# Optimization experiments

Hardware: AMD Instinct MI355X
Metric: run time of the kernel (lower is better)

Reference implementation:

```python
import jax, jax.numpy as jnp
import numpy as np

B, N, C, H, W = 2, 6, 64, 28, 50
D = 59  # len(arange(1.0, 60.0, 1.0))
BH, BW = 200, 200
BEV_X0, BEV_Y0 = -50.0, -50.0
RES_X, RES_Y = 0.5, 0.5  # (50-(-50))/200


def setup_inputs() -> dict:
    key = jax.random.key(0)
    k1, k2 = jax.random.split(key)
    features = jax.random.normal(k1, (B, N, C, H, W), dtype=jnp.float32)
    # depth distribution over D bins (softmax-normalized, as a depth net would emit)
    depth = jax.nn.softmax(jax.random.normal(k2, (B, N, D, H, W), dtype=jnp.float32), axis=2)
    # realistic pinhole intrinsics for a WxH feature map
    K = np.zeros((B, N, 3, 3), np.float32)
    K[..., 0, 0] = float(W)
    K[..., 1, 1] = float(W)
    K[..., 0, 2] = W / 2.0
    K[..., 1, 2] = H / 2.0
    K[..., 2, 2] = 1.0
    # cam-to-ego extrinsics: axis remap (z_cam->x_ego, x_cam->-y_ego, y_cam->-z_ego)
    # composed with a per-camera yaw, plus a small mounting translation
    R0 = np.array([[0, 0, 1], [-1, 0, 0], [0, -1, 0]], np.float32)
    E = np.zeros((B, N, 4, 4), np.float32)
    for n in range(N):
        yaw = 2.0 * np.pi * n / N
        Rz = np.array([[np.cos(yaw), -np.sin(yaw), 0.0],
                       [np.sin(yaw), np.cos(yaw), 0.0],
                       [0.0, 0.0, 1.0]], np.float32)
        E[:, n, :3, :3] = Rz @ R0
        E[:, n, 0, 3] = 1.5 * np.cos(yaw)
        E[:, n, 1, 3] = 1.5 * np.sin(yaw)
        E[:, n, 2, 3] = 1.6
    E[..., 3, 3] = 1.0
    return {
        "features": features,
        "depth": depth,
        "intrinsics": jnp.asarray(K),
        "extrinsics": jnp.asarray(E),
    }


def _frustum_ego(intrinsics, extrinsics):
    # pixel grid (H, W, 3) homogeneous coords
    xs = jnp.linspace(0.0, W - 1.0, W, dtype=jnp.float32)
    ys = jnp.linspace(0.0, H - 1.0, H, dtype=jnp.float32)
    yy, xx = jnp.meshgrid(ys, xs, indexing="ij")
    pix = jnp.stack([xx, yy, jnp.ones_like(xx)], axis=-1)  # (H, W, 3)
    depth_bins = jnp.arange(1.0, 60.0, 1.0, dtype=jnp.float32)  # (D,)
    frustum_cam = pix[None] * depth_bins[:, None, None, None]  # (D, H, W, 3)
    K_inv = jnp.linalg.inv(intrinsics)  # (B, N, 3, 3)
    cam = jnp.einsum("bnij,dhwj->bndhwi", K_inv, frustum_cam)  # (B, N, D, H, W, 3)
    R = extrinsics[..., :3, :3]
    t = extrinsics[..., :3, 3]
    ego = jnp.einsum("bnij,bndhwj->bndhwi", R, cam) + t[:, :, None, None, None, :]
    return ego


def reference(features, depth, intrinsics, extrinsics):
    ego = _frustum_ego(intrinsics, extrinsics)  # (B, N, D, H, W, 3)

    # lift: outer product of features (B,N,C,H,W) and depth (B,N,D,H,W)
    lifted = features[:, :, None] * depth[:, :, :, None]  # (B, N, D, C, H, W)
    lifted = lifted.transpose(0, 1, 2, 4, 5, 3).reshape(B, -1, C)  # b (n d h w) c

    fr = ego.reshape(B, -1, 3)  # b (n d h w) xyz
    x, y, z = fr[..., 0], fr[..., 1], fr[..., 2]
    # torch .long() truncates toward zero -> astype(int32) matches
    bx = ((x - BEV_X0) / RES_X).astype(jnp.int32)
    by = ((y - BEV_Y0) / RES_Y).astype(jnp.int32)
    valid = (bx >= 0) & (bx < BW) & (by >= 0) & (by < BH) & (z > 0)

    # flat scatter index with per-batch offset; invalid -> dummy segment (dropped)
    b_off = (jnp.arange(B, dtype=jnp.int32) * (BH * BW))[:, None]
    flat_idx = jnp.where(valid, b_off + by * BW + bx, B * BH * BW)
    seg = jax.ops.segment_sum(
        lifted.reshape(-1, C), flat_idx.reshape(-1), num_segments=B * BH * BW + 1
    )
    bev = seg[: B * BH * BW].reshape(B, BH, BW, C).transpose(0, 3, 1, 2)  # (B, C, BH, BW)
    return bev
```

## Files before the change

kernel.cpp:

```cpp
#include <hip/hip_runtime.h>
#include <hip/hip_bf16.h>

#define Bc 2
#define Nc 6
#define Cc 64
#define Hc 28
#define Wc 50
#define Dc 59
#define BHc 200
#define BWc 200

#define HWc (Hc * Wc)
#define NWAVES 8
#define DWAVE 8
#define NZ 640
#define ACC_ELEMS ((size_t)Bc * BHc * BWc * Cc)

__global__ __launch_bounds__(256) void fp_zero(float* __restrict__ acc)
{
    const size_t NF4 = ACC_ELEMS / 4;
    float4* a4 = (float4*)acc;
    size_t base = (size_t)blockIdx.x * 2048;
#pragma unroll
    for (int it = 0; it < 8; ++it) {
        size_t i = base + (size_t)it * 256 + threadIdx.x;
        if (i < NF4) a4[i] = make_float4(0.f, 0.f, 0.f, 0.f);
    }
}

__global__ __launch_bounds__(512) void fp_scatter6(
    const float* __restrict__ feats,
    const float* __restrict__ depth,
    const float* __restrict__ Kmat,
    const float* __restrict__ Emat,
    float* __restrict__ acc)
{
    __shared__ __align__(16) float feat_lds[Hc][Cc];

    int bid = blockIdx.x;
    int L   = (bid & 7) * 75 + (bid >> 3);
    int w   = L % Wc;
    int bn  = L / Wc;
    int b   = bn / Nc;
    int tid  = threadIdx.x;
    int lane = tid & 63;
    int wid  = tid >> 6;

    const size_t HW = (size_t)HWc;
    const float* fbase = feats + (size_t)bn * Cc * HW + w;
    const float* dcol  = depth + (size_t)bn * Dc * HW + w;

    for (int hh = wid; hh < Hc; hh += NWAVES)
        feat_lds[hh][lane] = fbase[(size_t)lane * HW + (size_t)hh * Wc];

    const float* K = Kmat + (size_t)bn * 9;
    float k00 = K[0], k01 = K[1], k02 = K[2];
    float k10 = K[3], k11 = K[4], k12 = K[5];
    float k20 = K[6], k21 = K[7], k22 = K[8];

    float c00 = __fsub_rn(__fmul_rn(k11, k22), __fmul_rn(k12, k21));
    float c01 = __fsub_rn(__fmul_rn(k12, k20), __fmul_rn(k10, k22));
    float c02 = __fsub_rn(__fmul_rn(k10, k21), __fmul_rn(k11, k20));
    float det = __fadd_rn(__fadd_rn(__fmul_rn(k00, c00), __fmul_rn(k01, c01)),
                          __fmul_rn(k02, c02));
    float i00 = __fdiv_rn(c00, det);
    float i01 = __fdiv_rn(__fsub_rn(__fmul_rn(k02, k21), __fmul_rn(k01, k22)), det);
    float i02 = __fdiv_rn(__fsub_rn(__fmul_rn(k01, k12), __fmul_rn(k02, k11)), det);
    float i10 = __fdiv_rn(c01, det);
    float i11 = __fdiv_rn(__fsub_rn(__fmul_rn(k00, k22), __fmul_rn(k02, k20)), det);
    float i12 = __fdiv_rn(__fsub_rn(__fmul_rn(k02, k10), __fmul_rn(k00, k12)), det);
    float i20 = __fdiv_rn(c02, det);
    float i21 = __fdiv_rn(__fsub_rn(__fmul_rn(k01, k20), __fmul_rn(k00, k21)), det);
    float i22 = __fdiv_rn(__fsub_rn(__fmul_rn(k00, k11), __fmul_rn(k01, k10)), det);

    const float* E = Emat + (size_t)bn * 16;
    float r00 = E[0], r01 = E[1], r02 = E[2],  tx = E[3];
    float r10 = E[4], r11 = E[5], r12 = E[6],  ty = E[7];
    float r20 = E[8], r21 = E[9], r22 = E[10], tz = E[11];

    __syncthreads();

    float* accb = acc + (size_t)b * (BHc * BWc) * Cc;

    int h = lane;
    float xf = (float)w;
    float yf = (float)h;

    float accv[DWAVE];
    float mval[DWAVE];
    int   prim[DWAVE];

#pragma unroll
    for (int k = 0; k < DWAVE; ++k) {
        accv[k] = 0.0f;
        mval[k] = 0.0f;
        prim[k] = -1;
        int dg = wid + NWAVES * k;
        if (dg < Dc) {
            float db = (float)(dg + 1);
            float dep = 0.0f;
            if (h < Hc)
                dep = dcol[(size_t)dg * HW + (size_t)h * Wc];

            float px = __fmul_rn(xf, db);
            float py = __fmul_rn(yf, db);
            float pz = db;

            float cx = __fadd_rn(__fadd_rn(__fmul_rn(i00, px), __fmul_rn(i01, py)), __fmul_rn(i02, pz));
            float cy = __fadd_rn(__fadd_rn(__fmul_rn(i10, px), __fmul_rn(i11, py)), __fmul_rn(i12, pz));
            float cz = __fadd_rn(__fadd_rn(__fmul_rn(i20, px), __fmul_rn(i21, py)), __fmul_rn(i22, pz));

            float ex = __fadd_rn(__fadd_rn(__fadd_rn(__fmul_rn(r00, cx), __fmul_rn(r01, cy)), __fmul_rn(r02, cz)), tx);
            float ey = __fadd_rn(__fadd_rn(__fadd_rn(__fmul_rn(r10, cx), __fmul_rn(r11, cy)), __fmul_rn(r12, cz)), ty);
            float ez = __fadd_rn(__fadd_rn(__fadd_rn(__fmul_rn(r20, cx), __fmul_rn(r21, cy)), __fmul_rn(r22, cz)), tz);

            int bx = (int)(__fmul_rn(__fadd_rn(ex, 50.0f), 2.0f));
            int by = (int)(__fmul_rn(__fadd_rn(ey, 50.0f), 2.0f));

            bool valid = (h < Hc) & (bx >= 0) & (bx < BWc) & (by >= 0) & (by < BHc) & (ez > 0.0f);
            int binidx = by * BWc + bx;

            unsigned long long vm = __ballot(valid);
            if (vm != 0ULL) {
                int first = __builtin_ctzll(vm);
                int pr = __shfl(binidx, first);
                unsigned long long match = __ballot(valid && (binidx == pr));
                unsigned long long rest  = vm & ~match;
                prim[k] = pr;
                mval[k] = (valid && (binidx == pr)) ? dep : 0.0f;

                while (rest) {
                    int hh2 = __builtin_ctzll(rest);
                    rest &= rest - 1;
                    int   bidx = __shfl(binidx, hh2);
                    float dv   = __shfl(dep, hh2);
                    atomicAdd(&accb[(size_t)bidx * Cc + lane],
                              __fmul_rn(feat_lds[hh2][lane], dv));
                }
            }
        }
    }

#pragma unroll
    for (int hh = 0; hh < Hc; ++hh) {
        float f = feat_lds[hh][lane];
#pragma unroll
        for (int k = 0; k < DWAVE; ++k) {
            float dk = __int_as_float(
                __builtin_amdgcn_readlane(__float_as_int(mval[k]), hh));
            accv[k] = __builtin_fmaf(f, dk, accv[k]);
        }
    }

#pragma unroll
    for (int k = 0; k < DWAVE; ++k) {
        if (prim[k] >= 0)
            atomicAdd(&accb[(size_t)prim[k] * Cc + lane], accv[k]);
    }
}

__global__ __launch_bounds__(256) void fp_transpose_kernel(
    const float* __restrict__ acc, float* __restrict__ out)
{
    __shared__ float tile[64][65];
    const int P = BHc * BWc;
    int b = blockIdx.y;
    int p0 = blockIdx.x * 64;
    int tx = threadIdx.x & 63;
    int ty = threadIdx.x >> 6;

    const float* src = acc + (size_t)b * P * Cc;
#pragma unroll
    for (int i = 0; i < 16; ++i) {
        int row = ty * 16 + i;
        tile[row][tx] = src[(size_t)(p0 + row) * Cc + tx];
    }
    __syncthreads();
    float* dst = out + (size_t)b * Cc * P;
#pragma unroll
    for (int i = 0; i < 16; ++i) {
        int c = ty * 16 + i;
        dst[(size_t)c * P + p0 + tx] = tile[tx][c];
    }
}

extern "C" void kernel_launch(void* const* d_in, const int* in_sizes, int n_in,
                              void* d_out, int out_size, void* d_ws, size_t ws_size,
                              hipStream_t stream) {
    const float* feats = (const float*)d_in[0];
    const float* depth = (const float*)d_in[1];
    const float* Kmat  = (const float*)d_in[2];
    const float* Emat  = (const float*)d_in[3];
    float* out = (float*)d_out;

    float* acc = (float*)d_ws;

    fp_zero<<<NZ, 256, 0, stream>>>(acc);

    fp_scatter6<<<600, 512, 0, stream>>>(feats, depth, Kmat, Emat, acc);

    fp_transpose_kernel<<<dim3((BHc * BWc) / 64, Bc), 256, 0, stream>>>(acc, out);
}
```

Baseline: 97.09 us.

## Exploit column-independent BEV bins to reduce over image rows before scattering

The scatter kernel is restructured so each block covers one camera and a pair of depth bins. It checks at runtime whether the intrinsics and extrinsics have zero yaw-cross terms. When they do, the BEV bin depends only on (w, d), so features times depth are summed over all rows in registers and a single atomic is issued per (w, d, channel). A general fallback still does a per-point atomic scatter. Features are staged per row pair in a swizzled LDS tile, which cuts atomic traffic but relies on an exact-zero matrix check that may not hold for most cameras (the yawed ones).

```diff
diff --git a/kernel.cpp b/kernel.cpp
--- a/kernel.cpp
+++ b/kernel.cpp
@@ -10,11 +10,11 @@
 #define BHc 200
 #define BWc 200
 
-#define HWc (Hc * Wc)
-#define NWAVES 8
-#define DWAVE 8
 #define NZ 640
 #define ACC_ELEMS ((size_t)Bc * BHc * BWc * Cc)
+#define DT 2
+#define NTILE 30
+#define NBLK (12 * NTILE)
 
 __global__ __launch_bounds__(256) void fp_zero(float* __restrict__ acc)
 {
@@ -28,134 +28,216 @@
     }
 }
 
-__global__ __launch_bounds__(512) void fp_scatter6(
+__global__ __launch_bounds__(256) void fp_fused(
     const float* __restrict__ feats,
     const float* __restrict__ depth,
     const float* __restrict__ Kmat,
     const float* __restrict__ Emat,
     float* __restrict__ acc)
 {
-    __shared__ __align__(16) float feat_lds[Hc][Cc];
-
-    int bid = blockIdx.x;
-    int L   = (bid & 7) * 75 + (bid >> 3);
-    int w   = L % Wc;
-    int bn  = L / Wc;
-    int b   = bn / Nc;
+    __shared__ __align__(16) float f_lds[2][64][64];
+    __shared__ float dep_lds[DT][Hc][52];
+
+    int bid  = blockIdx.x;
+    int xcd  = bid & 7;
+    int j    = bid >> 3;
+    int k    = (xcd & 1) * 45 + j;
+    int g    = xcd >> 1;
+    int bn   = 3 * g + k / 30;
+    int t    = k % 30;
+    int b    = bn / Nc;
+    int d0   = t * DT;
+
     int tid  = threadIdx.x;
     int lane = tid & 63;
-    int wid  = tid >> 6;
-
-    const size_t HW = (size_t)HWc;
-    const float* fbase = feats + (size_t)bn * Cc * HW + w;
-    const float* dcol  = depth + (size_t)bn * Dc * HW + w;
-
-    for (int hh = wid; hh < Hc; hh += NWAVES)
-        feat_lds[hh][lane] = fbase[(size_t)lane * HW + (size_t)hh * Wc];
+    int q    = tid >> 6;
+
+    const size_t HW = (size_t)Hc * Wc;
+    const float* Fb = feats + (size_t)bn * Cc * HW;
+    const float* Db = depth + (size_t)bn * Dc * HW;
+
+    for (int i = tid; i < (DT * Hc * Wc) / 2; i += 256) {
+        int dp  = i / 700;
+        int rem = i % 700;
+        int hh  = rem / 25;
+        int w2  = rem % 25;
+        int dg  = d0 + dp;
+        float2 v = make_float2(0.f, 0.f);
+        if (dg < Dc)
+            v = *(const float2*)(Db + ((size_t)dg * Hc + hh) * Wc + 2 * w2);
+        dep_lds[dp][hh][2 * w2]     = v.x;
+        dep_lds[dp][hh][2 * w2 + 1] = v.y;
+    }
 
     const float* K = Kmat + (size_t)bn * 9;
     float k00 = K[0], k01 = K[1], k02 = K[2];
     float k10 = K[3], k11 = K[4], k12 = K[5];
     float k20 = K[6], k21 = K[7], k22 = K[8];
-
-    float c00 = __fsub_rn(__fmul_rn(k11, k22), __fmul_rn(k12, k21));
-    float c01 = __fsub_rn(__fmul_rn(k12, k20), __fmul_rn(k10, k22));
-    float c02 = __fsub_rn(__fmul_rn(k10, k21), __fmul_rn(k11, k20));
-    float det = __fadd_rn(__fadd_rn(__fmul_rn(k00, c00), __fmul_rn(k01, c01)),
-                          __fmul_rn(k02, c02));
+    float c00 = __fsub_rn(__fmul_rn(k11,k22), __fmul_rn(k12,k21));
+    float c01 = __fsub_rn(__fmul_rn(k12,k20), __fmul_rn(k10,k22));
+    float c02 = __fsub_rn(__fmul_rn(k10,k21), __fmul_rn(k11,k20));
+    float det = __fadd_rn(__fadd_rn(__fmul_rn(k00,c00), __fmul_rn(k01,c01)), __fmul_rn(k02,c02));
     float i00 = __fdiv_rn(c00, det);
-    float i01 = __fdiv_rn(__fsub_rn(__fmul_rn(k02, k21), __fmul_rn(k01, k22)), det);
-    float i02 = __fdiv_rn(__fsub_rn(__fmul_rn(k01, k12), __fmul_rn(k02, k11)), det);
+    float i01 = __fdiv_rn(__fsub_rn(__fmul_rn(k02,k21), __fmul_rn(k01,k22)), det);
+    float i02 = __fdiv_rn(__fsub_rn(__fmul_rn(k01,k12), __fmul_rn(k02,k11)), det);
     float i10 = __fdiv_rn(c01, det);
-    float i11 = __fdiv_rn(__fsub_rn(__fmul_rn(k00, k22), __fmul_rn(k02, k20)), det);
-    float i12 = __fdiv_rn(__fsub_rn(__fmul_rn(k02, k10), __fmul_rn(k00, k12)), det);
+    float i11 = __fdiv_rn(__fsub_rn(__fmul_rn(k00,k22), __fmul_rn(k02,k20)), det);
+    float i12 = __fdiv_rn(__fsub_rn(__fmul_rn(k02,k10), __fmul_rn(k00,k12)), det);
     float i20 = __fdiv_rn(c02, det);
-    float i21 = __fdiv_rn(__fsub_rn(__fmul_rn(k01, k20), __fmul_rn(k00, k21)), det);
-    float i22 = __fdiv_rn(__fsub_rn(__fmul_rn(k00, k11), __fmul_rn(k01, k10)), det);
+    float i21 = __fdiv_rn(__fsub_rn(__fmul_rn(k01,k20), __fmul_rn(k00,k21)), det);
+    float i22 = __fdiv_rn(__fsub_rn(__fmul_rn(k00,k11), __fmul_rn(k01,k10)), det);
 
     const float* E = Emat + (size_t)bn * 16;
     float r00 = E[0], r01 = E[1], r02 = E[2],  tx = E[3];
     float r10 = E[4], r11 = E[5], r12 = E[6],  ty = E[7];
     float r20 = E[8], r21 = E[9], r22 = E[10], tz = E[11];
 
+    bool fast = (__float_as_uint(i01) == 0u) & (__float_as_uint(i10) == 0u) &
+                (__float_as_uint(i21) == 0u) & (__float_as_uint(r01) == 0u) &
+                (__float_as_uint(r11) == 0u) & (__float_as_uint(r20) == 0u) &
+                (__float_as_uint(r22) == 0u);
+
     __syncthreads();
 
     float* accb = acc + (size_t)b * (BHc * BWc) * Cc;
 
-    int h = lane;
-    float xf = (float)w;
-    float yf = (float)h;
-
-    float accv[DWAVE];
-    float mval[DWAVE];
-    int   prim[DWAVE];
-
-#pragma unroll
-    for (int k = 0; k < DWAVE; ++k) {
-        accv[k] = 0.0f;
-        mval[k] = 0.0f;
-        prim[k] = -1;
-        int dg = wid + NWAVES * k;
-        if (dg < Dc) {
+    int wblk[4];
+    wblk[0] = q; wblk[1] = q + 4; wblk[2] = q + 8; wblk[3] = (q == 0) ? 12 : 13;
+
+    float mval[DT][16];
+    {
+        int hl = (lane < Hc) ? lane : 0;
+#pragma unroll
+        for (int dp = 0; dp < DT; ++dp) {
+            int dg = d0 + dp;
             float db = (float)(dg + 1);
-            float dep = 0.0f;
-            if (h < Hc)
-                dep = dcol[(size_t)dg * HW + (size_t)h * Wc];
-
-            float px = __fmul_rn(xf, db);
-            float py = __fmul_rn(yf, db);
-            float pz = db;
-
-            float cx = __fadd_rn(__fadd_rn(__fmul_rn(i00, px), __fmul_rn(i01, py)), __fmul_rn(i02, pz));
-            float cy = __fadd_rn(__fadd_rn(__fmul_rn(i10, px), __fmul_rn(i11, py)), __fmul_rn(i12, pz));
-            float cz = __fadd_rn(__fadd_rn(__fmul_rn(i20, px), __fmul_rn(i21, py)), __fmul_rn(i22, pz));
-
-            float ex = __fadd_rn(__fadd_rn(__fadd_rn(__fmul_rn(r00, cx), __fmul_rn(r01, cy)), __fmul_rn(r02, cz)), tx);
-            float ey = __fadd_rn(__fadd_rn(__fadd_rn(__fmul_rn(r10, cx), __fmul_rn(r11, cy)), __fmul_rn(r12, cz)), ty);
-            float ez = __fadd_rn(__fadd_rn(__fadd_rn(__fmul_rn(r20, cx), __fmul_rn(r21, cy)), __fmul_rn(r22, cz)), tz);
-
-            int bx = (int)(__fmul_rn(__fadd_rn(ex, 50.0f), 2.0f));
-            int by = (int)(__fmul_rn(__fadd_rn(ey, 50.0f), 2.0f));
-
-            bool valid = (h < Hc) & (bx >= 0) & (bx < BWc) & (by >= 0) & (by < BHc) & (ez > 0.0f);
-            int binidx = by * BWc + bx;
-
-            unsigned long long vm = __ballot(valid);
-            if (vm != 0ULL) {
-                int first = __builtin_ctzll(vm);
-                int pr = __shfl(binidx, first);
-                unsigned long long match = __ballot(valid && (binidx == pr));
-                unsigned long long rest  = vm & ~match;
-                prim[k] = pr;
-                mval[k] = (valid && (binidx == pr)) ? dep : 0.0f;
-
-                while (rest) {
-                    int hh2 = __builtin_ctzll(rest);
-                    rest &= rest - 1;
-                    int   bidx = __shfl(binidx, hh2);
-                    float dv   = __shfl(dep, hh2);
-                    atomicAdd(&accb[(size_t)bidx * Cc + lane],
-                              __fmul_rn(feat_lds[hh2][lane], dv));
+            float py = __fmul_rn((float)lane, db);
+            float cy = __fadd_rn(__fadd_rn(__fmul_rn(i10, 0.0f), __fmul_rn(i11, py)), __fmul_rn(i12, db));
+            float ez = __fadd_rn(__fadd_rn(__fadd_rn(__fmul_rn(r20, 0.0f), __fmul_rn(r21, cy)), __fmul_rn(r22, 0.0f)), tz);
+            bool zok = (ez > 0.0f) && (dg < Dc);
+#pragma unroll
+            for (int s = 0; s < 16; ++s) {
+                int w = wblk[s >> 2] * 4 + (s & 3);
+                float dv = dep_lds[dp][hl][w];
+                mval[dp][s] = zok ? dv : 0.0f;
+            }
+        }
+    }
+
+    int binv = -1;
+    {
+        int p = lane;
+        if (p < 32) {
+            int s  = p >> 1;
+            int dp = p & 1;
+            int w  = wblk[s >> 2] * 4 + (s & 3);
+            int dg = d0 + dp;
+            if (w < Wc && dg < Dc) {
+                float db = (float)(dg + 1);
+                float px = __fmul_rn((float)w, db);
+                float pz = db;
+                float cx = __fadd_rn(__fadd_rn(__fmul_rn(i00, px), __fmul_rn(i01, 0.0f)), __fmul_rn(i02, pz));
+                float cz = __fadd_rn(__fadd_rn(__fmul_rn(i20, px), __fmul_rn(i21, 0.0f)), __fmul_rn(i22, pz));
+                float ex = __fadd_rn(__fadd_rn(__fadd_rn(__fmul_rn(r00, cx), __fmul_rn(r01, 0.0f)), __fmul_rn(r02, cz)), tx);
+                float ey = __fadd_rn(__fadd_rn(__fadd_rn(__fmul_rn(r10, cx), __fmul_rn(r11, 0.0f)), __fmul_rn(r12, cz)), ty);
+                int bx = (int)(__fmul_rn(__fadd_rn(ex, 50.0f), 2.0f));
+                int by = (int)(__fmul_rn(__fadd_rn(ey, 50.0f), 2.0f));
+                if (bx >= 0 && bx < BWc && by >= 0 && by < BHc)
+                    binv = by * BWc + bx;
+            }
+        }
+    }
+
+    float accv[DT][16];
+#pragma unroll
+    for (int dp = 0; dp < DT; ++dp)
+#pragma unroll
+        for (int s = 0; s < 16; ++s) accv[dp][s] = 0.0f;
+
+    for (int hc = 0; hc < 14; ++hc) {
+        __syncthreads();
+        for (int i = tid; i < 3200; i += 256) {
+            int c   = i / 50;
+            int rem = i % 50;
+            int hp  = rem >= 25;
+            int w2  = rem - hp * 25;
+            int w   = 2 * w2;
+            float2 v = *(const float2*)(Fb + ((size_t)c * Hc + hc * 2 + hp) * Wc + w);
+            int slot0 = ((w >> 2) ^ (c & 15));
+            f_lds[hp][c][slot0 * 4 + (w & 3)] = v.x;
+            int w1 = w + 1;
+            int slot1 = ((w1 >> 2) ^ (c & 15));
+            f_lds[hp][c][slot1 * 4 + (w1 & 3)] = v.y;
+        }
+        __syncthreads();
+
+        if (fast) {
+#pragma unroll
+            for (int hp = 0; hp < 2; ++hp) {
+                int h = hc * 2 + hp;
+#pragma unroll
+                for (int s4 = 0; s4 < 4; ++s4) {
+                    const float4 f4 = *(const float4*)&f_lds[hp][lane][(wblk[s4] ^ (lane & 15)) * 4];
+#pragma unroll
+                    for (int dp = 0; dp < DT; ++dp) {
+                        float d0v = __int_as_float(__builtin_amdgcn_readlane(__float_as_int(mval[dp][s4*4+0]), h));
+                        float d1v = __int_as_float(__builtin_amdgcn_readlane(__float_as_int(mval[dp][s4*4+1]), h));
+                        float d2v = __int_as_float(__builtin_amdgcn_readlane(__float_as_int(mval[dp][s4*4+2]), h));
+                        float d3v = __int_as_float(__builtin_amdgcn_readlane(__float_as_int(mval[dp][s4*4+3]), h));
+                        accv[dp][s4*4+0] = __builtin_fmaf(f4.x, d0v, accv[dp][s4*4+0]);
+                        accv[dp][s4*4+1] = __builtin_fmaf(f4.y, d1v, accv[dp][s4*4+1]);
+                        accv[dp][s4*4+2] = __builtin_fmaf(f4.z, d2v, accv[dp][s4*4+2]);
+                        accv[dp][s4*4+3] = __builtin_fmaf(f4.w, d3v, accv[dp][s4*4+3]);
+                    }
                 }
             }
-        }
-    }
-
-#pragma unroll
-    for (int hh = 0; hh < Hc; ++hh) {
-        float f = feat_lds[hh][lane];
-#pragma unroll
-        for (int k = 0; k < DWAVE; ++k) {
-            float dk = __int_as_float(
-                __builtin_amdgcn_readlane(__float_as_int(mval[k]), hh));
-            accv[k] = __builtin_fmaf(f, dk, accv[k]);
-        }
-    }
-
-#pragma unroll
-    for (int k = 0; k < DWAVE; ++k) {
-        if (prim[k] >= 0)
-            atomicAdd(&accb[(size_t)prim[k] * Cc + lane], accv[k]);
+        } else {
+            for (int hp = 0; hp < 2; ++hp) {
+                int h = hc * 2 + hp;
+                float yf = (float)h;
+                for (int s = 0; s < 16; ++s) {
+                    int w = wblk[s >> 2] * 4 + (s & 3);
+                    if (w >= Wc) continue;
+                    float xf = (float)w;
+                    const float4 f4 = *(const float4*)&f_lds[hp][lane][(wblk[s >> 2] ^ (lane & 15)) * 4];
+                    float fv = (s & 3) == 0 ? f4.x : (s & 3) == 1 ? f4.y : (s & 3) == 2 ? f4.z : f4.w;
+                    for (int dp = 0; dp < DT; ++dp) {
+                        int dg = d0 + dp;
+                        if (dg >= Dc) continue;
+                        float db = (float)(dg + 1);
+                        float px = __fmul_rn(xf, db);
+                        float py = __fmul_rn(yf, db);
+                        float pz = db;
+                        float cx = __fadd_rn(__fadd_rn(__fmul_rn(i00,px), __fmul_rn(i01,py)), __fmul_rn(i02,pz));
+                        float cy = __fadd_rn(__fadd_rn(__fmul_rn(i10,px), __fmul_rn(i11,py)), __fmul_rn(i12,pz));
+                        float cz = __fadd_rn(__fadd_rn(__fmul_rn(i20,px), __fmul_rn(i21,py)), __fmul_rn(i22,pz));
+                        float ex = __fadd_rn(__fadd_rn(__fadd_rn(__fmul_rn(r00,cx), __fmul_rn(r01,cy)), __fmul_rn(r02,cz)), tx);
+                        float ey = __fadd_rn(__fadd_rn(__fadd_rn(__fmul_rn(r10,cx), __fmul_rn(r11,cy)), __fmul_rn(r12,cz)), ty);
+                        float ez = __fadd_rn(__fadd_rn(__fadd_rn(__fmul_rn(r20,cx), __fmul_rn(r21,cy)), __fmul_rn(r22,cz)), tz);
+                        int bx = (int)(__fmul_rn(__fadd_rn(ex, 50.0f), 2.0f));
+                        int by = (int)(__fmul_rn(__fadd_rn(ey, 50.0f), 2.0f));
+                        if (bx >= 0 && bx < BWc && by >= 0 && by < BHc && ez > 0.0f) {
+                            float dv = dep_lds[dp][h][w];
+                            atomicAdd(&accb[(size_t)(by * BWc + bx) * Cc + lane],
+                                      __fmul_rn(fv, dv));
+                        }
+                    }
+                }
+            }
+        }
+    }
+
+    if (fast) {
+#pragma unroll
+        for (int s = 0; s < 16; ++s) {
+#pragma unroll
+            for (int dp = 0; dp < DT; ++dp) {
+                int p = s * 2 + dp;
+                int sbin = __builtin_amdgcn_readlane(binv, p);
+                if (sbin >= 0)
+                    atomicAdd(&accb[(size_t)sbin * Cc + lane], accv[dp][s]);
+            }
+        }
     }
 }
 
@@ -192,12 +274,9 @@
     const float* Kmat  = (const float*)d_in[2];
     const float* Emat  = (const float*)d_in[3];
     float* out = (float*)d_out;
-
     float* acc = (float*)d_ws;
 
     fp_zero<<<NZ, 256, 0, stream>>>(acc);
-
-    fp_scatter6<<<600, 512, 0, stream>>>(feats, depth, Kmat, Emat, acc);
-
+    fp_fused<<<NBLK, 256, 0, stream>>>(feats, depth, Kmat, Emat, acc);
     fp_transpose_kernel<<<dim3((BHc * BWc) / 64, Bc), 256, 0, stream>>>(acc, out);
 }
```

After: 148.6 us. 1.53x slower.

## Tile scatter blocks over four columns and half depth with LDS-staged inputs

Applied to the files above, without the earlier changes.

Each block of the scatter kernel now covers four image columns and half of the depth bins. Eight waves split as four columns by two depth sub-ranges, and each wave handles fifteen depth bins. Features and depth values are staged into shared memory with float2 loads, replacing the single-column strided global reads, and the block count drops from 600 to 312. The aim is to cut poorly coalesced global traffic. The cost is larger per-thread register arrays and fewer blocks, which may lower occupancy and parallelism.

```diff
diff --git a/kernel.cpp b/kernel.cpp
--- a/kernel.cpp
+++ b/kernel.cpp
@@ -10,11 +10,13 @@
 #define BHc 200
 #define BWc 200
 
-#define HWc (Hc * Wc)
-#define NWAVES 8
-#define DWAVE 8
 #define NZ 640
 #define ACC_ELEMS ((size_t)Bc * BHc * BWc * Cc)
+
+#define W4N 13
+#define DH 30
+#define KPW 15
+#define NBLK (12 * W4N * 2)
 
 __global__ __launch_bounds__(256) void fp_zero(float* __restrict__ acc)
 {
@@ -28,50 +30,80 @@
     }
 }
 
-__global__ __launch_bounds__(512) void fp_scatter6(
+__global__ __launch_bounds__(512) void fp_scatter7(
     const float* __restrict__ feats,
     const float* __restrict__ depth,
     const float* __restrict__ Kmat,
     const float* __restrict__ Emat,
     float* __restrict__ acc)
 {
-    __shared__ __align__(16) float feat_lds[Hc][Cc];
+    __shared__ float f_lds[Hc][4][65];
+    __shared__ float d_lds[DH][4][29];
 
     int bid = blockIdx.x;
-    int L   = (bid & 7) * 75 + (bid >> 3);
-    int w   = L % Wc;
-    int bn  = L / Wc;
+    int lin = (bid & 7) * 39 + (bid >> 3);
+    int bn    = lin / 26;
+    int rest  = lin % 26;
+    int w4    = rest >> 1;
+    int dhalf = rest & 1;
     int b   = bn / Nc;
+    int w0  = w4 * 4;
+    int d0h = dhalf * DH;
+
     int tid  = threadIdx.x;
     int lane = tid & 63;
     int wid  = tid >> 6;
 
-    const size_t HW = (size_t)HWc;
-    const float* fbase = feats + (size_t)bn * Cc * HW + w;
-    const float* dcol  = depth + (size_t)bn * Dc * HW + w;
-
-    for (int hh = wid; hh < Hc; hh += NWAVES)
-        feat_lds[hh][lane] = fbase[(size_t)lane * HW + (size_t)hh * Wc];
+    const size_t HW = (size_t)Hc * Wc;
+    const float* Fb = feats + (size_t)bn * Cc * HW;
+    const float* Db = depth + (size_t)bn * Dc * HW;
+
+    for (int i = tid; i < Cc * Hc * 2; i += 512) {
+        int c  = i / 56;
+        int j2 = i % 56;
+        int hh = j2 >> 1;
+        int p  = j2 & 1;
+        int w  = w0 + 2 * p;
+        if (w + 1 < Wc) {
+            float2 v = *(const float2*)(Fb + ((size_t)c * Hc + hh) * Wc + w);
+            f_lds[hh][2 * p][c]     = v.x;
+            f_lds[hh][2 * p + 1][c] = v.y;
+        } else if (w < Wc) {
+            f_lds[hh][2 * p][c] = Fb[((size_t)c * Hc + hh) * Wc + w];
+        }
+    }
+
+    for (int i = tid; i < DH * Hc * 2; i += 512) {
+        int dp = i / 56;
+        int j2 = i % 56;
+        int hh = j2 >> 1;
+        int p  = j2 & 1;
+        int dg = d0h + dp;
+        int w  = w0 + 2 * p;
+        if (dg < Dc && w + 1 < Wc) {
+            float2 v = *(const float2*)(Db + ((size_t)dg * Hc + hh) * Wc + w);
+            d_lds[dp][2 * p][hh]     = v.x;
+            d_lds[dp][2 * p + 1][hh] = v.y;
+        }
+    }
 
     const float* K = Kmat + (size_t)bn * 9;
     float k00 = K[0], k01 = K[1], k02 = K[2];
     float k10 = K[3], k11 = K[4], k12 = K[5];
     float k20 = K[6], k21 = K[7], k22 = K[8];
-
-    float c00 = __fsub_rn(__fmul_rn(k11, k22), __fmul_rn(k12, k21));
-    float c01 = __fsub_rn(__fmul_rn(k12, k20), __fmul_rn(k10, k22));
-    float c02 = __fsub_rn(__fmul_rn(k10, k21), __fmul_rn(k11, k20));
-    float det = __fadd_rn(__fadd_rn(__fmul_rn(k00, c00), __fmul_rn(k01, c01)),
-                          __fmul_rn(k02, c02));
+    float c00 = __fsub_rn(__fmul_rn(k11,k22), __fmul_rn(k12,k21));
+    float c01 = __fsub_rn(__fmul_rn(k12,k20), __fmul_rn(k10,k22));
+    float c02 = __fsub_rn(__fmul_rn(k10,k21), __fmul_rn(k11,k20));
+    float det = __fadd_rn(__fadd_rn(__fmul_rn(k00,c00), __fmul_rn(k01,c01)), __fmul_rn(k02,c02));
     float i00 = __fdiv_rn(c00, det);
-    float i01 = __fdiv_rn(__fsub_rn(__fmul_rn(k02, k21), __fmul_rn(k01, k22)), det);
-    float i02 = __fdiv_rn(__fsub_rn(__fmul_rn(k01, k12), __fmul_rn(k02, k11)), det);
+    float i01 = __fdiv_rn(__fsub_rn(__fmul_rn(k02,k21), __fmul_rn(k01,k22)), det);
+    float i02 = __fdiv_rn(__fsub_rn(__fmul_rn(k01,k12), __fmul_rn(k02,k11)), det);
     float i10 = __fdiv_rn(c01, det);
-    float i11 = __fdiv_rn(__fsub_rn(__fmul_rn(k00, k22), __fmul_rn(k02, k20)), det);
-    float i12 = __fdiv_rn(__fsub_rn(__fmul_rn(k02, k10), __fmul_rn(k00, k12)), det);
+    float i11 = __fdiv_rn(__fsub_rn(__fmul_rn(k00,k22), __fmul_rn(k02,k20)), det);
+    float i12 = __fdiv_rn(__fsub_rn(__fmul_rn(k02,k10), __fmul_rn(k00,k12)), det);
     float i20 = __fdiv_rn(c02, det);
-    float i21 = __fdiv_rn(__fsub_rn(__fmul_rn(k01, k20), __fmul_rn(k00, k21)), det);
-    float i22 = __fdiv_rn(__fsub_rn(__fmul_rn(k00, k11), __fmul_rn(k01, k10)), det);
+    float i21 = __fdiv_rn(__fsub_rn(__fmul_rn(k01,k20), __fmul_rn(k00,k21)), det);
+    float i22 = __fdiv_rn(__fsub_rn(__fmul_rn(k00,k11), __fmul_rn(k01,k10)), det);
 
     const float* E = Emat + (size_t)bn * 16;
     float r00 = E[0], r01 = E[1], r02 = E[2],  tx = E[3];
@@ -82,25 +114,30 @@
 
     float* accb = acc + (size_t)b * (BHc * BWc) * Cc;
 
+    int wp   = wid >> 1;
+    int dsub = wid & 1;
+    int w    = w0 + wp;
+    bool active = (w < Wc);
+
     int h = lane;
     float xf = (float)w;
     float yf = (float)h;
-
-    float accv[DWAVE];
-    float mval[DWAVE];
-    int   prim[DWAVE];
-
-#pragma unroll
-    for (int k = 0; k < DWAVE; ++k) {
+    int hl = (lane < Hc) ? lane : (Hc - 1);
+
+    float accv[KPW];
+    float mval[KPW];
+    int   prim[KPW];
+
+#pragma unroll
+    for (int k = 0; k < KPW; ++k) {
         accv[k] = 0.0f;
         mval[k] = 0.0f;
         prim[k] = -1;
-        int dg = wid + NWAVES * k;
-        if (dg < Dc) {
+        int ld = dsub * KPW + k;
+        int dg = d0h + ld;
+        if (active && dg < Dc) {
             float db = (float)(dg + 1);
-            float dep = 0.0f;
-            if (h < Hc)
-                dep = dcol[(size_t)dg * HW + (size_t)h * Wc];
+            float dep = (h < Hc) ? d_lds[ld][wp][hl] : 0.0f;
 
             float px = __fmul_rn(xf, db);
             float py = __fmul_rn(yf, db);
@@ -125,17 +162,17 @@
                 int first = __builtin_ctzll(vm);
                 int pr = __shfl(binidx, first);
                 unsigned long long match = __ballot(valid && (binidx == pr));
-                unsigned long long rest  = vm & ~match;
+                unsigned long long rest2 = vm & ~match;
                 prim[k] = pr;
                 mval[k] = (valid && (binidx == pr)) ? dep : 0.0f;
 
-                while (rest) {
-                    int hh2 = __builtin_ctzll(rest);
-                    rest &= rest - 1;
+                while (rest2) {
+                    int hh2 = __builtin_ctzll(rest2);
+                    rest2 &= rest2 - 1;
                     int   bidx = __shfl(binidx, hh2);
                     float dv   = __shfl(dep, hh2);
                     atomicAdd(&accb[(size_t)bidx * Cc + lane],
-                              __fmul_rn(feat_lds[hh2][lane], dv));
+                              __fmul_rn(f_lds[hh2][wp][lane], dv));
                 }
             }
         }
@@ -143,9 +180,9 @@
 
 #pragma unroll
     for (int hh = 0; hh < Hc; ++hh) {
-        float f = feat_lds[hh][lane];
-#pragma unroll
-        for (int k = 0; k < DWAVE; ++k) {
+        float f = f_lds[hh][wp][lane];
+#pragma unroll
+        for (int k = 0; k < KPW; ++k) {
             float dk = __int_as_float(
                 __builtin_amdgcn_readlane(__float_as_int(mval[k]), hh));
             accv[k] = __builtin_fmaf(f, dk, accv[k]);
@@ -153,7 +190,7 @@
     }
 
 #pragma unroll
-    for (int k = 0; k < DWAVE; ++k) {
+    for (int k = 0; k < KPW; ++k) {
         if (prim[k] >= 0)
             atomicAdd(&accb[(size_t)prim[k] * Cc + lane], accv[k]);
     }
@@ -192,12 +229,9 @@
     const float* Kmat  = (const float*)d_in[2];
     const float* Emat  = (const float*)d_in[3];
     float* out = (float*)d_out;
-
     float* acc = (float*)d_ws;
 
     fp_zero<<<NZ, 256, 0, stream>>>(acc);
-
-    fp_scatter6<<<600, 512, 0, stream>>>(feats, depth, Kmat, Emat, acc);
-
+    fp_scatter7<<<NBLK, 512, 0, stream>>>(feats, depth, Kmat, Emat, acc);
     fp_transpose_kernel<<<dim3((BHc * BWc) / 64, Bc), 256, 0, stream>>>(acc, out);
 }
```

Result: slower. 102.3 us (+5.4%).
